# Optimization experiments

Measured on AMD Instinct MI355X. Metric: run time of the kernel, lower is better.

Reference implementation:

```python
import jax, jax.numpy as jnp
import numpy as np

SCALE = 2
EPS = 1e-5  # BatchNorm2d default eps


def conv1x1(x, W, b):
    # x: [B,C,H,W], W: [O,C], b: [O]
    return jnp.einsum('bchw,oc->bohw', x, W) + b[None, :, None, None]


def maxpool(x, s):
    B, C, H, W = x.shape
    return x.reshape(B, C, H // s, s, W // s, s).max(axis=(3, 5))


def upsample_bilinear_ac(x, s):
    # bilinear upsample, align_corners=True
    B, C, H, W = x.shape
    Ho, Wo = H * s, W * s
    ys = jnp.arange(Ho) * ((H - 1) / (Ho - 1))
    xs = jnp.arange(Wo) * ((W - 1) / (Wo - 1))
    y0 = jnp.floor(ys).astype(jnp.int32)
    y1 = jnp.minimum(y0 + 1, H - 1)
    wy = (ys - y0).astype(x.dtype)
    x0 = jnp.floor(xs).astype(jnp.int32)
    x1 = jnp.minimum(x0 + 1, W - 1)
    wx = (xs - x0).astype(x.dtype)
    rows = x[:, :, y0, :] * (1 - wy)[None, None, :, None] + x[:, :, y1, :] * wy[None, None, :, None]
    return rows[:, :, :, x0] * (1 - wx) + rows[:, :, :, x1] * wx


def setup_inputs() -> dict:
    key = jax.random.key(0)
    ks = jax.random.split(key, 9)
    B, Cin, Cm, dk, H, W = 4, 64, 64, 64, 128, 128
    return {
        'x': jax.random.normal(ks[0], (B, Cin, H, W), jnp.float32),
        'memory': jax.random.normal(ks[1], (B, Cm, H, W), jnp.float32),
        'W_qkv': jax.random.normal(ks[2], (3 * dk, Cm), jnp.float32) * 0.05,
        'b_qkv': jax.random.normal(ks[3], (3 * dk,), jnp.float32) * 0.05,
        'W_out': jax.random.normal(ks[4], (Cin, dk), jnp.float32) * 0.05,
        'b_out': jax.random.normal(ks[5], (Cin,), jnp.float32) * 0.05,
        'bn_gamma': jax.random.uniform(ks[6], (Cin,), jnp.float32, 0.5, 1.5),
        'bn_beta': jax.random.normal(ks[7], (Cin,), jnp.float32) * 0.05,
        'gamma': jax.random.normal(ks[8], (1,), jnp.float32) * 0.1,
    }


def reference(x, memory, W_qkv, b_qkv, W_out, b_out, bn_gamma, bn_beta, gamma):
    d_k = W_qkv.shape[0] // 3
    qkv = conv1x1(memory, W_qkv, b_qkv)
    qkv = maxpool(qkv, SCALE)
    q, k, v = jnp.split(qkv, 3, axis=1)
    B, C, H, W = v.shape
    q = q.reshape(B, C, H * W).transpose(0, 2, 1)  # [B,N,C]
    k = k.reshape(B, C, H * W)                      # [B,C,N]
    v = v.reshape(B, C, H * W).transpose(0, 2, 1)   # [B,N,C]
    scale = jnp.asarray(d_k, x.dtype) ** 0.5
    attn = jax.nn.softmax(jnp.einsum('bnc,bcm->bnm', q, k) / scale, axis=-1)
    S = jnp.einsum('bnm,bmc->bnc', attn, v).transpose(0, 2, 1).reshape(B, C, H, W)
    S = upsample_bilinear_ac(S, SCALE)
    S = conv1x1(S, W_out, b_out)
    # BatchNorm2d (training mode: biased batch stats over B,H,W)
    mean = S.mean(axis=(0, 2, 3), keepdims=True)
    var = S.var(axis=(0, 2, 3), keepdims=True)
    S = (S - mean) / jnp.sqrt(var + EPS) * bn_gamma[None, :, None, None] + bn_beta[None, :, None, None]
    return x + gamma[0] * S
```

## Files before the change

kernel.cpp:

```cpp
#include <hip/hip_runtime.h>
#include <stdint.h>

typedef unsigned short u16;
typedef unsigned int   u32;
typedef __attribute__((ext_vector_type(8))) __bf16 bf16x8;
typedef __attribute__((ext_vector_type(4))) float  f32x4;
typedef __attribute__((ext_vector_type(2))) float  f32x2;
typedef __attribute__((ext_vector_type(4))) u32    u32x4;
typedef __attribute__((ext_vector_type(2))) u32    u32x2;

#define QSCALE 0.18033688011112042f

__device__ __forceinline__ u16 f2bf(float x) {
  u32 u = __builtin_bit_cast(u32, x);
  u = (u + 0x7FFFu + ((u >> 16) & 1u)) >> 16;
  return (u16)u;
}

__device__ __forceinline__ u32 cvt_pk_bf16(float lo, float hi) {
  u32 r;
  asm("v_cvt_pk_bf16_f32 %0, %1, %2" : "=v"(r) : "v"(lo), "v"(hi));
  return r;
}

__global__ __launch_bounds__(512) void k_qkvpool(
    const float* __restrict__ mem, const float* __restrict__ Wqkv,
    const float* __restrict__ bqkv, const float* __restrict__ Wout,
    u16* __restrict__ Q, u16* __restrict__ K, u16* __restrict__ V,
    float* __restrict__ stats)
{
  const int oy = blockIdx.x, b = blockIdx.y, t = threadIdx.x;
  const int w = t >> 6, l4 = t & 15, lh = (t >> 4) & 3;
  const int wq = w & 3, wp = w >> 2;

  if (oy == 0 && b == 0 && t < 128) stats[t] = 0.f;

  __shared__ __align__(16) u16 lds[49152];
  u16* mlds  = lds;
  u16* wlds  = lds + 16384;
  u16* qlds  = lds + 28672;
  u16* klds  = lds + 32768;
  u16* vldsT = lds + 36864;
  u16* wolds = lds + 40960;
  u16* vplds = lds + 45056;

  float bias[3][4];
  #pragma unroll
  for (int j = 0; j < 3; ++j)
    #pragma unroll
    for (int r = 0; r < 4; ++r) {
      int oc = wq * 48 + 16 * j + lh * 4 + r;
      float bv = bqkv[oc];
      bias[j][r] = (oc < 64) ? bv * QSCALE : bv;
    }

  {
    const float* src = mem + ((size_t)b * 64) * 16384 + 2 * oy * 128;
    #pragma unroll
    for (int i = 0; i < 8; ++i) {
      int g = t + 512 * i;
      int px = g & 255, c0 = (g >> 8) * 4;
      float f0 = src[(size_t)(c0 + 0) * 16384 + px];
      float f1 = src[(size_t)(c0 + 1) * 16384 + px];
      float f2 = src[(size_t)(c0 + 2) * 16384 + px];
      float f3 = src[(size_t)(c0 + 3) * 16384 + px];
      u32x2 pk;
      pk[0] = (u32)f2bf(f0) | ((u32)f2bf(f1) << 16);
      pk[1] = (u32)f2bf(f2) | ((u32)f2bf(f3) << 16);
      *(u32x2*)(mlds + px * 64 + (((c0 * 2) ^ ((px & 7) << 4)) >> 1)) = pk;
    }
  }
  {
    #pragma unroll
    for (int i = 0; i < 6; ++i) {
      int g = t + 512 * i;
      int oc = g >> 4, c0 = (g & 15) * 4;
      f32x4 wv = *(const f32x4*)(Wqkv + oc * 64 + c0);
      u32x2 pk;
      pk[0] = (u32)f2bf(wv[0]) | ((u32)f2bf(wv[1]) << 16);
      pk[1] = (u32)f2bf(wv[2]) | ((u32)f2bf(wv[3]) << 16);
      *(u32x2*)(wlds + oc * 64 + (((c0 * 2) ^ ((oc & 7) << 4)) >> 1)) = pk;
    }
  }
  {
    #pragma unroll
    for (int i = 0; i < 2; ++i) {
      int g = t + 512 * i;
      int oc = g >> 4, c0 = (g & 15) * 4;
      f32x4 wv = *(const f32x4*)(Wout + oc * 64 + c0);
      u32x2 pk;
      pk[0] = (u32)f2bf(wv[0]) | ((u32)f2bf(wv[1]) << 16);
      pk[1] = (u32)f2bf(wv[2]) | ((u32)f2bf(wv[3]) << 16);
      *(u32x2*)(wolds + oc * 64 + (((c0 * 2) ^ ((oc & 7) << 4)) >> 1)) = pk;
    }
  }
  __syncthreads();

  const int sw  = (l4 & 7) << 4;
  const int oF0 = ((lh * 16) ^ sw) >> 1;
  const int oF1 = ((64 + lh * 16) ^ sw) >> 1;
  bf16x8 af[3][2];
  #pragma unroll
  for (int j = 0; j < 3; ++j) {
    const u16* ar = wlds + (wq * 48 + 16 * j + l4) * 64;
    af[j][0] = *(const bf16x8*)(ar + oF0);
    af[j][1] = *(const bf16x8*)(ar + oF1);
  }

  #pragma unroll 2
  for (int tpi = 0; tpi < 4; ++tpi) {
    const int tp = wp * 4 + tpi;
    const u16* br0 = mlds + (16 * tp + l4) * 64;
    const u16* br1 = mlds + (128 + 16 * tp + l4) * 64;
    bf16x8 b00 = *(const bf16x8*)(br0 + oF0);
    bf16x8 b01 = *(const bf16x8*)(br0 + oF1);
    bf16x8 b10 = *(const bf16x8*)(br1 + oF0);
    bf16x8 b11 = *(const bf16x8*)(br1 + oF1);
    const int ox = 8 * tp + (l4 >> 1);
    #pragma unroll
    for (int j = 0; j < 3; ++j) {
      f32x4 a0 = {0, 0, 0, 0}, a1 = {0, 0, 0, 0};
      a0 = __builtin_amdgcn_mfma_f32_16x16x32_bf16(af[j][0], b00, a0, 0, 0, 0);
      a0 = __builtin_amdgcn_mfma_f32_16x16x32_bf16(af[j][1], b01, a0, 0, 0, 0);
      a1 = __builtin_amdgcn_mfma_f32_16x16x32_bf16(af[j][0], b10, a1, 0, 0, 0);
      a1 = __builtin_amdgcn_mfma_f32_16x16x32_bf16(af[j][1], b11, a1, 0, 0, 0);
      const int ocj = wq * 48 + 16 * j;
      const float sc = (ocj < 64) ? QSCALE : 1.0f;
      #pragma unroll
      for (int r = 0; r < 4; ++r) {
        float m = fmaxf(a0[r], a1[r]);
        m = fmaxf(m, __shfl_xor(m, 1, 64));
        u16 val = f2bf(m * sc + bias[j][r]);
        if ((l4 & 1) == 0) {
          int oc = ocj + lh * 4 + r;
          if (ocj < 64)       qlds[ox * 64 + oc]        = val;
          else if (ocj < 128) klds[ox * 64 + (oc - 64)] = val;
          else {
            int vch = oc - 128;
            vldsT[ox * 64 + (((vch * 2) ^ ((ox & 7) << 4)) >> 1)] = val;
          }
        }
      }
    }
  }
  __syncthreads();

  {
    const u16* ar = wolds + (wq * 16 + l4) * 64;
    bf16x8 aw0 = *(const bf16x8*)(ar + oF0);
    bf16x8 aw1 = *(const bf16x8*)(ar + oF1);
    #pragma unroll
    for (int nti = 0; nti < 2; ++nti) {
      const int nt = wp * 2 + nti;
      const u16* brow = vldsT + (nt * 16 + l4) * 64;
      bf16x8 bw0 = *(const bf16x8*)(brow + oF0);
      bf16x8 bw1 = *(const bf16x8*)(brow + oF1);
      f32x4 u = {0, 0, 0, 0};
      u = __builtin_amdgcn_mfma_f32_16x16x32_bf16(aw0, bw0, u, 0, 0, 0);
      u = __builtin_amdgcn_mfma_f32_16x16x32_bf16(aw1, bw1, u, 0, 0, 0);
      #pragma unroll
      for (int r = 0; r < 4; ++r) {
        int oc = wq * 16 + lh * 4 + r;
        vplds[oc * 64 + nt * 16 + l4] = f2bf(u[r]);
      }
    }
  }
  __syncthreads();

  {
    int r = t >> 3, e8 = (t & 7) * 8;
    size_t nb = (size_t)oy * 64;
    *(u32x4*)(Q + ((size_t)b * 4096 + nb + r) * 64 + e8) = *(const u32x4*)(qlds + r * 64 + e8);
    *(u32x4*)(K + ((size_t)b * 4096 + nb + r) * 64 + e8) = *(const u32x4*)(klds + r * 64 + e8);
    *(u32x4*)(V + ((size_t)b * 64 + r) * 4096 + nb + e8) = *(const u32x4*)(vplds + r * 64 + e8);
  }
}

__global__ __launch_bounds__(1024, 4) void k_attn(
    const u16* __restrict__ Q, const u16* __restrict__ K,
    const u16* __restrict__ V, const float* __restrict__ bo,
    float* __restrict__ Sa)
{
  const int qb = blockIdx.x, b = blockIdx.y, t = threadIdx.x;
  const int w = t >> 6, l4 = t & 15, lh = (t >> 4) & 3;
  const int sgrp = w >> 2, wq = w & 3;

  __shared__ __align__(16) u16 kvbuf[16384 + 18432];

  u16* kt_w = kvbuf + sgrp * 4096;
  u16* vt_w = kvbuf + 16384 + sgrp * 4608;

  const int qrow = qb * 64 + wq * 16 + l4;
  const u16* qp = Q + ((size_t)b * 4096 + qrow) * 64 + lh * 8;
  bf16x8 qa0 = *(const bf16x8*)qp;
  bf16x8 qa1 = *(const bf16x8*)(qp + 32);

  f32x4 ot[4] = {{0,0,0,0},{0,0,0,0},{0,0,0,0},{0,0,0,0}};
  float lr = 0.f;

  const int tl = t & 255;
  const int skr = tl >> 2, skc = tl & 3;
  const u16* kgp = K + ((size_t)b * 4096 + sgrp * 1024 + skr) * 64 + skc * 16;
  const u16* vgp = V + ((size_t)b * 64 + skr) * 4096 + sgrp * 1024 + skc * 16;
  const u32 fbw = (u32)(((skr & 3) | (((skr >> 3) & 1) << 2)) << 4);
  u16* kwp0 = kt_w + skr * 64 + ((((u32)(skc * 32))      ^ fbw) >> 1);
  u16* kwp1 = kt_w + skr * 64 + ((((u32)(skc * 32 + 16)) ^ fbw) >> 1);
  u16* vwp  = vt_w + skr * 72 + skc * 16;

  const int rbase = ((l4 >> 2) << 3) + (l4 & 3);
  const int fbr   = ((l4 & 3) | (((l4 >> 2) & 1) << 2)) << 4;
  const int offL  = ((lh * 16) ^ fbr) >> 1;
  const int offH  = offL ^ 32;

  u32x4 rk0 = *(const u32x4*)kgp;
  u32x4 rk1 = *(const u32x4*)(kgp + 8);
  u32x4 rv0 = *(const u32x4*)vgp;
  u32x4 rv1 = *(const u32x4*)(vgp + 8);

  #pragma unroll 1
  for (int kti = 0; kti < 16; ++kti) {
    *(u32x4*)kwp0 = rk0;
    *(u32x4*)kwp1 = rk1;
    *(u32x4*)vwp = rv0;
    *(u32x4*)(vwp + 8) = rv1;
    __syncthreads();

    if (kti < 15) {
      rk0 = *(const u32x4*)(kgp + (kti + 1) * 4096);
      rk1 = *(const u32x4*)(kgp + (kti + 1) * 4096 + 8);
      rv0 = *(const u32x4*)(vgp + (kti + 1) * 64);
      rv1 = *(const u32x4*)(vgp + (kti + 1) * 64 + 8);
    }

    #pragma unroll
    for (int ss = 0; ss < 2; ++ss) {
      const u16* kr0 = kt_w + (ss * 32 + rbase) * 64;
      const u16* kr1 = kr0 + 4 * 64;
      bf16x8 vf0 = *(const bf16x8*)(vt_w + (l4)      * 72 + ss * 32 + lh * 8);
      bf16x8 vf1 = *(const bf16x8*)(vt_w + (16 + l4) * 72 + ss * 32 + lh * 8);
      bf16x8 vf2 = *(const bf16x8*)(vt_w + (32 + l4) * 72 + ss * 32 + lh * 8);
      bf16x8 vf3 = *(const bf16x8*)(vt_w + (48 + l4) * 72 + ss * 32 + lh * 8);
      bf16x8 k00 = *(const bf16x8*)(kr0 + offL);
      bf16x8 k01 = *(const bf16x8*)(kr0 + offH);
      bf16x8 k10 = *(const bf16x8*)(kr1 + offL);
      bf16x8 k11 = *(const bf16x8*)(kr1 + offH);

      f32x4 s0 = {0, 0, 0, 0}, s1 = {0, 0, 0, 0};
      s0 = __builtin_amdgcn_mfma_f32_16x16x32_bf16(k00, qa0, s0, 0, 0, 0);
      s0 = __builtin_amdgcn_mfma_f32_16x16x32_bf16(k01, qa1, s0, 0, 0, 0);
      s1 = __builtin_amdgcn_mfma_f32_16x16x32_bf16(k10, qa0, s1, 0, 0, 0);
      s1 = __builtin_amdgcn_mfma_f32_16x16x32_bf16(k11, qa1, s1, 0, 0, 0);

      float p0[4], p1[4];
      #pragma unroll
      for (int r = 0; r < 4; ++r) {
        p0[r] = exp2f(s0[r]);
        p1[r] = exp2f(s1[r]);
        lr += p0[r] + p1[r];
      }
      u32x4 pw;
      pw[0] = cvt_pk_bf16(p0[0], p0[1]);
      pw[1] = cvt_pk_bf16(p0[2], p0[3]);
      pw[2] = cvt_pk_bf16(p1[0], p1[1]);
      pw[3] = cvt_pk_bf16(p1[2], p1[3]);
      bf16x8 pf = __builtin_bit_cast(bf16x8, pw);

      ot[0] = __builtin_amdgcn_mfma_f32_16x16x32_bf16(vf0, pf, ot[0], 0, 0, 0);
      ot[1] = __builtin_amdgcn_mfma_f32_16x16x32_bf16(vf1, pf, ot[1], 0, 0, 0);
      ot[2] = __builtin_amdgcn_mfma_f32_16x16x32_bf16(vf2, pf, ot[2], 0, 0, 0);
      ot[3] = __builtin_amdgcn_mfma_f32_16x16x32_bf16(vf3, pf, ot[3], 0, 0, 0);
    }
    __syncthreads();
  }

  lr += __shfl_xor(lr, 16, 64);
  lr += __shfl_xor(lr, 32, 64);

  float* opb = (float*)kvbuf;
  float* mlb = (float*)(kvbuf + 32768);
  #pragma unroll
  for (int d = 0; d < 4; ++d)
    #pragma unroll
    for (int r = 0; r < 4; ++r)
      opb[w * 1024 + (16 * d + lh * 4 + r) * 16 + l4] = ot[d][r];
  if (lh == 0) mlb[w * 16 + l4] = lr;
  __syncthreads();

  const int ch = t >> 4, q0v = (t & 15) * 4;
  const float bout_c = bo[ch];
  f32x4 res;
  #pragma unroll
  for (int j = 0; j < 4; ++j) {
    int q = q0v + j, wq2 = q >> 4, ql = q & 15;
    float L = mlb[(wq2)*16      + ql] + mlb[(4 + wq2)*16  + ql]
            + mlb[(8 + wq2)*16  + ql] + mlb[(12 + wq2)*16 + ql];
    float O = opb[(wq2)*1024      + ch * 16 + ql]
            + opb[(4 + wq2)*1024  + ch * 16 + ql]
            + opb[(8 + wq2)*1024  + ch * 16 + ql]
            + opb[(12 + wq2)*1024 + ch * 16 + ql];
    res[j] = O / L + bout_c;
  }
  *(f32x4*)(Sa + ((size_t)b * 64 + ch) * 4096 + (size_t)qb * 64 + q0v) = res;
}

__global__ __launch_bounds__(1024) void k_stats(const float* __restrict__ U,
                                                float* __restrict__ stats)
{
  const int c = blockIdx.x & 63, b = blockIdx.x >> 6, t = threadIdx.x;
  __shared__ __align__(16) float up[4096];
  __shared__ float red[32];
  *(f32x4*)&up[t * 4] = *(const f32x4*)(U + ((size_t)b * 64 + c) * 4096 + t * 4);
  __syncthreads();
  const float R = 0.49606299212598425f;
  float sum = 0.f, ssq = 0.f;
  #pragma unroll 4
  for (int i = 0; i < 16; ++i) {
    int px = t + 1024 * i;
    int yo = px >> 7, xo = px & 127;
    float ys = yo * R; int y0 = (int)ys; float wy = ys - y0; int y1 = min(y0 + 1, 63);
    float xs = xo * R; int x0 = (int)xs; float wx = xs - x0; int x1 = min(x0 + 1, 63);
    const float* r0 = up + y0 * 64; const float* r1 = up + y1 * 64;
    float v0 = r0[x0] * (1.f - wx) + r0[x1] * wx;
    float v1 = r1[x0] * (1.f - wx) + r1[x1] * wx;
    float v = v0 * (1.f - wy) + v1 * wy;
    sum += v; ssq += v * v;
  }
  #pragma unroll
  for (int d = 32; d >= 1; d >>= 1) {
    sum += __shfl_down(sum, d, 64);
    ssq += __shfl_down(ssq, d, 64);
  }
  if ((t & 63) == 0) { red[t >> 6] = sum; red[16 + (t >> 6)] = ssq; }
  __syncthreads();
  if (t == 0) {
    float s = 0.f, q = 0.f;
    #pragma unroll
    for (int i = 0; i < 16; ++i) { s += red[i]; q += red[16 + i]; }
    atomicAdd(&stats[c], s);
    atomicAdd(&stats[64 + c], q);
  }
}

__global__ __launch_bounds__(1024) void k_apply(
    const float* __restrict__ U, const float* __restrict__ stats,
    const float* __restrict__ x, const float* __restrict__ bng,
    const float* __restrict__ bnb, const float* __restrict__ gam,
    float* __restrict__ out)
{
  const int c = blockIdx.x & 63, b = blockIdx.x >> 6, t = threadIdx.x;
  __shared__ __align__(16) float up[4096];
  *(f32x4*)&up[t * 4] = *(const f32x4*)(U + ((size_t)b * 64 + c) * 4096 + t * 4);
  __syncthreads();
  const float inv = 1.0f / 65536.0f;
  float mean = stats[c] * inv;
  float var  = stats[64 + c] * inv - mean * mean;
  float rsig = rsqrtf(var + 1e-5f);
  float g = gam[0];
  float A  = g * bng[c] * rsig;
  float Bc = g * (bnb[c] - mean * rsig * bng[c]);
  const float R = 0.49606299212598425f;
  const size_t base = ((size_t)b * 64 + c) * 16384;
  #pragma unroll 4
  for (int i = 0; i < 16; ++i) {
    int px = t + 1024 * i;
    int yo = px >> 7, xo = px & 127;
    float ys = yo * R; int y0 = (int)ys; float wy = ys - y0; int y1 = min(y0 + 1, 63);
    float xs = xo * R; int x0 = (int)xs; float wx = xs - x0; int x1 = min(x0 + 1, 63);
    const float* r0 = up + y0 * 64; const float* r1 = up + y1 * 64;
    float v0 = r0[x0] * (1.f - wx) + r0[x1] * wx;
    float v1 = r1[x0] * (1.f - wx) + r1[x1] * wx;
    float v = v0 * (1.f - wy) + v1 * wy;
    out[base + px] = x[base + px] + v * A + Bc;
  }
}

extern "C" void kernel_launch(void* const* d_in, const int* in_sizes, int n_in,
                              void* d_out, int out_size, void* d_ws, size_t ws_size,
                              hipStream_t stream)
{
  const float* x      = (const float*)d_in[0];
  const float* memory = (const float*)d_in[1];
  const float* Wqkv   = (const float*)d_in[2];
  const float* bqkv   = (const float*)d_in[3];
  const float* Wout   = (const float*)d_in[4];
  const float* bout   = (const float*)d_in[5];
  const float* bng    = (const float*)d_in[6];
  const float* bnb    = (const float*)d_in[7];
  const float* gamma  = (const float*)d_in[8];

  char* ws = (char*)d_ws;
  u16*   Q     = (u16*)(ws + 0);
  u16*   Kk    = (u16*)(ws + (2u << 20));
  u16*   Vt    = (u16*)(ws + (4u << 20));
  float* U     = (float*)(ws + (10u << 20));
  float* stats = (float*)(ws + (14u << 20));
  float* out   = (float*)d_out;

  k_qkvpool<<<dim3(64, 4), 512, 0, stream>>>(memory, Wqkv, bqkv, Wout, Q, Kk, Vt, stats);
  k_attn   <<<dim3(64, 4), 1024, 0, stream>>>(Q, Kk, Vt, bout, U);
  k_stats  <<<256, 1024, 0, stream>>>(U, stats);
  k_apply  <<<256, 1024, 0, stream>>>(U, stats, x, bng, bnb, gamma, out);
}
```

Baseline: 61.71 us.

## Split attention into 32-query blocks with XCD-aware block mapping

The attention kernel now runs 512 blocks of 512 threads, each handling 32 queries instead of 64. Each block keeps four key-split groups, each group with two query waves. Blocks are mapped so that all blocks of one batch land on the same pair of XCDs, which aims to improve L2 reuse of that batch's K and V. This doubles the grid to fill more CUs, at the cost of each K/V tile being loaded by twice as many blocks and each thread issuing more global loads.

```diff
diff --git a/kernel.cpp b/kernel.cpp
--- a/kernel.cpp
+++ b/kernel.cpp
@@ -176,21 +176,24 @@
   }
 }
 
-__global__ __launch_bounds__(1024, 4) void k_attn(
+__global__ __launch_bounds__(512) void k_attn(
     const u16* __restrict__ Q, const u16* __restrict__ K,
     const u16* __restrict__ V, const float* __restrict__ bo,
     float* __restrict__ Sa)
 {
-  const int qb = blockIdx.x, b = blockIdx.y, t = threadIdx.x;
+  const int bid = blockIdx.x, t = threadIdx.x;
+  const int xcd = bid & 7;
+  const int b   = xcd >> 1;
+  const int qb  = ((bid >> 3) << 1) | (xcd & 1);
   const int w = t >> 6, l4 = t & 15, lh = (t >> 4) & 3;
-  const int sgrp = w >> 2, wq = w & 3;
+  const int sgrp = w >> 1, wq = w & 1;
 
   __shared__ __align__(16) u16 kvbuf[16384 + 18432];
 
   u16* kt_w = kvbuf + sgrp * 4096;
   u16* vt_w = kvbuf + 16384 + sgrp * 4608;
 
-  const int qrow = qb * 64 + wq * 16 + l4;
+  const int qrow = qb * 32 + wq * 16 + l4;
   const u16* qp = Q + ((size_t)b * 4096 + qrow) * 64 + lh * 8;
   bf16x8 qa0 = *(const bf16x8*)qp;
   bf16x8 qa1 = *(const bf16x8*)(qp + 32);
@@ -198,14 +201,16 @@
   f32x4 ot[4] = {{0,0,0,0},{0,0,0,0},{0,0,0,0},{0,0,0,0}};
   float lr = 0.f;
 
-  const int tl = t & 255;
-  const int skr = tl >> 2, skc = tl & 3;
-  const u16* kgp = K + ((size_t)b * 4096 + sgrp * 1024 + skr) * 64 + skc * 16;
-  const u16* vgp = V + ((size_t)b * 64 + skr) * 4096 + sgrp * 1024 + skc * 16;
+  const int tl = t & 127;
+  const int skr = tl >> 1, hf = tl & 1;
+  const u16* kgp = K + ((size_t)b * 4096 + sgrp * 1024 + skr) * 64 + hf * 32;
+  const u16* vgp = V + ((size_t)b * 64 + skr) * 4096 + sgrp * 1024 + hf * 32;
   const u32 fbw = (u32)(((skr & 3) | (((skr >> 3) & 1) << 2)) << 4);
-  u16* kwp0 = kt_w + skr * 64 + ((((u32)(skc * 32))      ^ fbw) >> 1);
-  u16* kwp1 = kt_w + skr * 64 + ((((u32)(skc * 32 + 16)) ^ fbw) >> 1);
-  u16* vwp  = vt_w + skr * 72 + skc * 16;
+  u16* kwp0 = kt_w + skr * 64 + ((((u32)(hf * 64))      ^ fbw) >> 1);
+  u16* kwp1 = kt_w + skr * 64 + ((((u32)(hf * 64 + 16)) ^ fbw) >> 1);
+  u16* kwp2 = kt_w + skr * 64 + ((((u32)(hf * 64 + 32)) ^ fbw) >> 1);
+  u16* kwp3 = kt_w + skr * 64 + ((((u32)(hf * 64 + 48)) ^ fbw) >> 1);
+  u16* vwp  = vt_w + skr * 72 + hf * 32;
 
   const int rbase = ((l4 >> 2) << 3) + (l4 & 3);
   const int fbr   = ((l4 & 3) | (((l4 >> 2) & 1) << 2)) << 4;
@@ -214,22 +219,34 @@
 
   u32x4 rk0 = *(const u32x4*)kgp;
   u32x4 rk1 = *(const u32x4*)(kgp + 8);
+  u32x4 rk2 = *(const u32x4*)(kgp + 16);
+  u32x4 rk3 = *(const u32x4*)(kgp + 24);
   u32x4 rv0 = *(const u32x4*)vgp;
   u32x4 rv1 = *(const u32x4*)(vgp + 8);
+  u32x4 rv2 = *(const u32x4*)(vgp + 16);
+  u32x4 rv3 = *(const u32x4*)(vgp + 24);
 
   #pragma unroll 1
   for (int kti = 0; kti < 16; ++kti) {
     *(u32x4*)kwp0 = rk0;
     *(u32x4*)kwp1 = rk1;
+    *(u32x4*)kwp2 = rk2;
+    *(u32x4*)kwp3 = rk3;
     *(u32x4*)vwp = rv0;
-    *(u32x4*)(vwp + 8) = rv1;
+    *(u32x4*)(vwp + 8)  = rv1;
+    *(u32x4*)(vwp + 16) = rv2;
+    *(u32x4*)(vwp + 24) = rv3;
     __syncthreads();
 
     if (kti < 15) {
       rk0 = *(const u32x4*)(kgp + (kti + 1) * 4096);
       rk1 = *(const u32x4*)(kgp + (kti + 1) * 4096 + 8);
+      rk2 = *(const u32x4*)(kgp + (kti + 1) * 4096 + 16);
+      rk3 = *(const u32x4*)(kgp + (kti + 1) * 4096 + 24);
       rv0 = *(const u32x4*)(vgp + (kti + 1) * 64);
       rv1 = *(const u32x4*)(vgp + (kti + 1) * 64 + 8);
+      rv2 = *(const u32x4*)(vgp + (kti + 1) * 64 + 16);
+      rv3 = *(const u32x4*)(vgp + (kti + 1) * 64 + 24);
     }
 
     #pragma unroll
@@ -277,7 +294,7 @@
   lr += __shfl_xor(lr, 32, 64);
 
   float* opb = (float*)kvbuf;
-  float* mlb = (float*)(kvbuf + 32768);
+  float* mlb = (float*)(kvbuf + 16384);
   #pragma unroll
   for (int d = 0; d < 4; ++d)
     #pragma unroll
@@ -286,21 +303,28 @@
   if (lh == 0) mlb[w * 16 + l4] = lr;
   __syncthreads();
 
-  const int ch = t >> 4, q0v = (t & 15) * 4;
+  const int ch = t >> 3, qq = t & 7;
+  const int q0 = qq * 4;
+  const int wq2 = q0 >> 4, ql = q0 & 15;
   const float bout_c = bo[ch];
+  f32x4 Osum = {0, 0, 0, 0};
+  float Ls[4];
+  #pragma unroll
+  for (int j = 0; j < 4; ++j) Ls[j] = 0.f;
+  #pragma unroll
+  for (int s = 0; s < 4; ++s) {
+    const int pw_ = 2 * s + wq2;
+    f32x4 Ov = *(const f32x4*)&opb[pw_ * 1024 + ch * 16 + ql];
+    #pragma unroll
+    for (int j = 0; j < 4; ++j) {
+      Osum[j] += Ov[j];
+      Ls[j]   += mlb[pw_ * 16 + ql + j];
+    }
+  }
   f32x4 res;
   #pragma unroll
-  for (int j = 0; j < 4; ++j) {
-    int q = q0v + j, wq2 = q >> 4, ql = q & 15;
-    float L = mlb[(wq2)*16      + ql] + mlb[(4 + wq2)*16  + ql]
-            + mlb[(8 + wq2)*16  + ql] + mlb[(12 + wq2)*16 + ql];
-    float O = opb[(wq2)*1024      + ch * 16 + ql]
-            + opb[(4 + wq2)*1024  + ch * 16 + ql]
-            + opb[(8 + wq2)*1024  + ch * 16 + ql]
-            + opb[(12 + wq2)*1024 + ch * 16 + ql];
-    res[j] = O / L + bout_c;
-  }
-  *(f32x4*)(Sa + ((size_t)b * 64 + ch) * 4096 + (size_t)qb * 64 + q0v) = res;
+  for (int j = 0; j < 4; ++j) res[j] = Osum[j] / Ls[j] + bout_c;
+  *(f32x4*)(Sa + ((size_t)b * 64 + ch) * 4096 + (size_t)qb * 32 + q0) = res;
 }
 
 __global__ __launch_bounds__(1024) void k_stats(const float* __restrict__ U,
@@ -397,7 +421,7 @@
   float* out   = (float*)d_out;
 
   k_qkvpool<<<dim3(64, 4), 512, 0, stream>>>(memory, Wqkv, bqkv, Wout, Q, Kk, Vt, stats);
-  k_attn   <<<dim3(64, 4), 1024, 0, stream>>>(Q, Kk, Vt, bout, U);
+  k_attn   <<<512, 512, 0, stream>>>(Q, Kk, Vt, bout, U);
   k_stats  <<<256, 1024, 0, stream>>>(U, stats);
   k_apply  <<<256, 1024, 0, stream>>>(U, stats, x, bng, bnb, gamma, out);
 }
```

Result: slower. 71.04 us (+15.1%).
